# Optimization experiments

Measured on AMD Instinct MI355X. Metric: run time of the kernel, lower is better.

The kernel has to match this reference:

```python
import jax, jax.numpy as jnp
import numpy as np

N_HEAD = 8
D_MODEL = 512
D_K = 512
D_V = 512
D_KH = D_K // N_HEAD
D_VH = D_V // N_HEAD
EPS = 1e-6


def setup_inputs() -> dict:
    key = jax.random.key(0)
    ks = jax.random.split(key, 10)
    B, L = 16, 1024
    q = jax.random.normal(ks[0], (B, L, D_MODEL), dtype=jnp.float32)
    k = jax.random.normal(ks[1], (B, L, D_MODEL), dtype=jnp.float32)
    v = jax.random.normal(ks[2], (B, L, D_MODEL), dtype=jnp.float32)
    mask = jax.random.randint(ks[3], (B, L, L), 0, 2).astype(bool)
    s = 1.0 / np.sqrt(D_MODEL)
    Wq = jax.random.normal(ks[4], (D_MODEL, D_K), dtype=jnp.float32) * s
    Wk = jax.random.normal(ks[5], (D_MODEL, D_K), dtype=jnp.float32) * s
    Wv = jax.random.normal(ks[6], (D_MODEL, D_V), dtype=jnp.float32) * s
    Wfc = jax.random.normal(ks[7], (D_V, D_MODEL), dtype=jnp.float32) * (1.0 / np.sqrt(D_V))
    gamma = jnp.ones((D_MODEL,), dtype=jnp.float32)
    beta = jnp.zeros((D_MODEL,), dtype=jnp.float32)
    return {"q": q, "k": k, "v": v, "mask": mask, "Wq": Wq, "Wk": Wk,
            "Wv": Wv, "Wfc": Wfc, "gamma": gamma, "beta": beta}


def reference(q, k, v, mask, Wq, Wk, Wv, Wfc, gamma, beta):
    B, Lq, _ = q.shape
    Lk = k.shape[1]
    residual = q
    # projections -> [B, H, L, d_head]
    qh = (q @ Wq).reshape(B, Lq, N_HEAD, D_KH).transpose(0, 2, 1, 3)
    kh = (k @ Wk).reshape(B, Lk, N_HEAD, D_KH).transpose(0, 2, 1, 3)
    vh = (v @ Wv).reshape(B, Lk, N_HEAD, D_VH).transpose(0, 2, 1, 3)
    # scaled dot-product attention; scale uses per-head dim (source rebinds d_k)
    scores = jnp.einsum('bhqd,bhkd->bhqk', qh / np.sqrt(D_KH), kh)
    scores = jnp.where(mask[:, None, :, :], -1e9, scores)
    attn = jax.nn.softmax(scores, axis=-1)
    out = jnp.einsum('bhqk,bhkd->bhqd', attn, vh)
    out = out.transpose(0, 2, 1, 3).reshape(B, Lq, D_V)
    out = out @ Wfc + residual
    # layer norm
    mu = jnp.mean(out, axis=-1, keepdims=True)
    var = jnp.var(out, axis=-1, keepdims=True)
    out = (out - mu) * jax.lax.rsqrt(var + EPS) * gamma + beta
    return out, attn
```

## Files before the change

kernel.cpp:

```cpp
#include <hip/hip_runtime.h>
#include <hip/hip_bf16.h>

typedef __attribute__((ext_vector_type(8))) short s8v;
typedef __attribute__((ext_vector_type(4))) short s4v;
typedef __attribute__((ext_vector_type(4))) float f4v;

__device__ __forceinline__ short f2bf(float f){
  unsigned u = __builtin_bit_cast(unsigned, f);
  u += 0x7fffu + ((u >> 16) & 1u);
  return (short)(u >> 16);
}

__device__ __forceinline__ f4v mfma16(s8v a, s8v b, f4v c){
  return __builtin_amdgcn_mfma_f32_16x16x32_bf16(a, b, c, 0, 0, 0);
}

__device__ __forceinline__ void ldsbar(){
  asm volatile("s_waitcnt lgkmcnt(0)" ::: "memory");
  __builtin_amdgcn_s_barrier();
  __builtin_amdgcn_sched_barrier(0);
}

__global__ __launch_bounds__(256) void prep_kernel(
    const int* __restrict__ mask, unsigned* __restrict__ bits,
    const float* __restrict__ Wq, const float* __restrict__ Wk,
    const float* __restrict__ Wv, const float* __restrict__ Wfc,
    short* __restrict__ Wt)
{
  if (blockIdx.x < 2048){
    const int lane = threadIdx.x & 63;
    const int wid = blockIdx.x*4 + (threadIdx.x >> 6);
    for (int i = 0; i < 32; ++i){
      const int c = wid*32 + i;
      int mv = __builtin_nontemporal_load(&mask[(size_t)c*64 + lane]);
      unsigned long long bal = __ballot(mv != 0);
      if (lane == 0)  bits[c*2]   = (unsigned)bal;
      if (lane == 32) bits[c*2+1] = (unsigned)(bal >> 32);
    }
  } else {
    const int bid = blockIdx.x - 2048;
    const int w = bid >> 10;
    const float* __restrict__ W = (w==0)?Wq:(w==1)?Wk:(w==2)?Wv:Wfc;
    const int idx = (bid & 1023)*256 + threadIdx.x;
    const int kk = idx >> 9, n = idx & 511;
    Wt[w*262144 + n*512 + kk] = f2bf(W[idx]);
  }
}

__global__ __launch_bounds__(256) void proj_kernel(
    const float* __restrict__ qin, const float* __restrict__ kin,
    const float* __restrict__ vin, const short* __restrict__ Wt,
    short* __restrict__ Qh, short* __restrict__ Kh, short* __restrict__ Vt)
{
  const int work = (blockIdx.x & 7)*384 + (blockIdx.x >> 3);
  const int z = work >> 10;
  const int r = work & 1023;
  const int mt = r >> 2, nt = r & 3;
  const float* __restrict__ A = (z==0) ? qin : (z==1) ? kin : vin;
  const short* __restrict__ W = Wt + z*262144;
  const int m0 = mt*64, n0 = nt*128;
  __shared__ __align__(16) short Alds[64*40];
  __shared__ __align__(16) short Tlds[128*68];
  const int tid = threadIdx.x, lane = tid & 63, wave = tid >> 6;
  const int wm = wave >> 1, wn = wave & 1;
  const int col = lane & 15, kg = lane >> 4;
  f4v acc[2][4];
  #pragma unroll
  for (int i=0;i<2;i++)
    #pragma unroll
    for (int j=0;j<4;j++) acc[i][j] = (f4v){0.f,0.f,0.f,0.f};

  const int arow = tid >> 2, aoff = (tid & 3)*8;
  const float* Ap = A + (size_t)(m0 + arow)*512 + aoff;
  short* Aw = &Alds[arow*40 + aoff];

  float4 x0 = *(const float4*)(Ap);
  float4 x1 = *(const float4*)(Ap + 4);

  for (int k0 = 0; k0 < 512; k0 += 32){
    s8v ab;
    ab[0]=f2bf(x0.x); ab[1]=f2bf(x0.y); ab[2]=f2bf(x0.z); ab[3]=f2bf(x0.w);
    ab[4]=f2bf(x1.x); ab[5]=f2bf(x1.y); ab[6]=f2bf(x1.z); ab[7]=f2bf(x1.w);
    ldsbar();
    *(s8v*)Aw = ab;
    if (k0 < 480){
      x0 = *(const float4*)(Ap + k0 + 32);
      x1 = *(const float4*)(Ap + k0 + 36);
    }
    ldsbar();
    s8v af0 = *(const s8v*)&Alds[(wm*32 + col)*40 + kg*8];
    s8v af1 = *(const s8v*)&Alds[(wm*32 + 16 + col)*40 + kg*8];
    #pragma unroll
    for (int f=0; f<4; f++){
      const int n = n0 + wn*64 + f*16 + col;
      s8v bf = *(const s8v*)(W + n*512 + k0 + kg*8);
      acc[0][f] = mfma16(af0, bf, acc[0][f]);
      acc[1][f] = mfma16(af1, bf, acc[1][f]);
    }
  }

  if (z < 2){
    const float scale = (z==0) ? 0.125f : 1.0f;
    short* D = (z==0) ? Qh : Kh;
    #pragma unroll
    for (int fr=0; fr<2; fr++)
      #pragma unroll
      for (int f=0; f<4; f++)
        #pragma unroll
        for (int j=0; j<4; j++){
          int rr = m0 + wm*32 + fr*16 + kg*4 + j;
          int c = n0 + wn*64 + f*16 + col;
          int b = rr >> 10, l = rr & 1023, hh = c >> 6, d = c & 63;
          D[((size_t)(b*8+hh)*1024 + l)*64 + d] = f2bf(acc[fr][f][j] * scale);
        }
  } else {
    ldsbar();
    #pragma unroll
    for (int fr=0; fr<2; fr++)
      #pragma unroll
      for (int f=0; f<4; f++)
        #pragma unroll
        for (int j=0; j<4; j++){
          const int rl = wm*32 + fr*16 + kg*4 + j;
          const int cl = wn*64 + f*16 + col;
          Tlds[cl*68 + rl] = f2bf(acc[fr][f][j]);
        }
    ldsbar();
    const int b = m0 >> 10, lbase = m0 & 1023;
    #pragma unroll
    for (int it=0; it<4; ++it){
      const int idx = it*256 + tid;
      const int cl = idx >> 3, rc = idx & 7;
      const int c = n0 + cl, hh = c >> 6, d = c & 63;
      s8v vv = *(const s8v*)&Tlds[cl*68 + rc*8];
      *(s8v*)(Vt + ((size_t)(b*8+hh)*64 + d)*1024 + lbase + rc*8) = vv;
    }
  }
}

__global__ __launch_bounds__(256) void attn_kernel(
  const short* __restrict__ Qh, const short* __restrict__ Kh,
  const short* __restrict__ Vt, const unsigned* __restrict__ bits,
  float* __restrict__ attn, short* __restrict__ ctx)
{
  const int work = ((blockIdx.x & 7) << 8) | (blockIdx.x >> 3);
  const int bh = work >> 4;
  const int q0 = (work & 15) * 64;
  const int b = bh >> 3, h = bh & 7;
  __shared__ unsigned mb[64*33];
  __shared__ __align__(16) short Pb[64*128];
  __shared__ float red[256];
  __shared__ float rowinv[64];
  const int tid = threadIdx.x, lane = tid & 63, wave = tid >> 6;
  const int col = lane & 15, kg = lane >> 4;
  const short* Qb = Qh + (size_t)bh*65536;
  const short* Kb = Kh + (size_t)bh*65536;
  const short* Vb = Vt + (size_t)bh*65536;
  const f4v zf = (f4v){0.f,0.f,0.f,0.f};

  {
    const int r = tid >> 2, w = (tid & 3)*8;
    const unsigned* src = bits + (size_t)(b*1024 + q0 + r)*32 + w;
    uint4 w0 = *(const uint4*)src;
    uint4 w1 = *(const uint4*)(src + 4);
    unsigned* dst = &mb[r*33 + w];
    dst[0]=w0.x; dst[1]=w0.y; dst[2]=w0.z; dst[3]=w0.w;
    dst[4]=w1.x; dst[5]=w1.y; dst[6]=w1.z; dst[7]=w1.w;
  }

  s8v qf[4][2];
  #pragma unroll
  for (int qi = 0; qi < 4; ++qi)
    #pragma unroll
    for (int ks = 0; ks < 2; ++ks)
      qf[qi][ks] = *(const s8v*)(Qb + (q0 + qi*16 + col)*64 + ks*32 + kg*8);

  __syncthreads();

  float sum[4] = {0.f, 0.f, 0.f, 0.f};
  for (int it = 0; it < 8; ++it){
    const int c0 = it*128 + wave*32;
    unsigned mw[4];
    #pragma unroll
    for (int qi = 0; qi < 4; ++qi) mw[qi] = mb[(qi*16 + col)*33 + (c0>>5)];
    #pragma unroll
    for (int ch = 0; ch < 2; ++ch){
      const short* kp = Kb + (c0 + ch*16 + col)*64 + kg*8;
      s8v kf0 = *(const s8v*)kp;
      s8v kf1 = *(const s8v*)(kp + 32);
      #pragma unroll
      for (int qi = 0; qi < 4; ++qi){
        f4v a = mfma16(kf0, qf[qi][0], zf);
        a = mfma16(kf1, qf[qi][1], a);
        #pragma unroll
        for (int j = 0; j < 4; ++j){
          const int bit = ch*16 + kg*4 + j;
          float e = __expf(a[j]);
          sum[qi] += ((mw[qi]>>bit)&1) ? 0.f : e;
        }
      }
    }
  }
  #pragma unroll
  for (int qi = 0; qi < 4; ++qi){
    sum[qi] += __shfl_xor(sum[qi], 16);
    sum[qi] += __shfl_xor(sum[qi], 32);
  }
  if (kg == 0){
    #pragma unroll
    for (int qi = 0; qi < 4; ++qi) red[wave*64 + qi*16 + col] = sum[qi];
  }
  __syncthreads();
  if (tid < 64)
    rowinv[tid] = 1.0f / (red[tid] + red[64+tid] + red[128+tid] + red[192+tid]);
  __syncthreads();
  float inv[4];
  #pragma unroll
  for (int qi = 0; qi < 4; ++qi) inv[qi] = rowinv[qi*16 + col];

  f4v cacc[4] = {zf, zf, zf, zf};
  const int d0 = wave*16;
  float* ab = attn + (size_t)(bh*1024 + q0)*1024;
  const int sw = (col & 7) << 3;
  for (int it = 0; it < 8; ++it){
    const int c0 = it*128 + wave*32;
    unsigned mw[4];
    #pragma unroll
    for (int qi = 0; qi < 4; ++qi) mw[qi] = mb[(qi*16 + col)*33 + (c0>>5)];
    #pragma unroll
    for (int ch = 0; ch < 2; ++ch){
      const int cc = c0 + ch*16;
      const short* kp = Kb + (cc + col)*64 + kg*8;
      s8v kf0 = *(const s8v*)kp;
      s8v kf1 = *(const s8v*)(kp + 32);
      #pragma unroll
      for (int qi = 0; qi < 4; ++qi){
        f4v a = mfma16(kf0, qf[qi][0], zf);
        a = mfma16(kf1, qf[qi][1], a);
        f4v p; s4v pk;
        #pragma unroll
        for (int j = 0; j < 4; ++j){
          const int bit = ch*16 + kg*4 + j;
          float e = __expf(a[j]) * inv[qi];
          p[j] = ((mw[qi]>>bit)&1) ? 0.f : e;
          pk[j] = f2bf(p[j]);
        }
        __builtin_nontemporal_store(p,
            (f4v*)(ab + (size_t)(qi*16 + col)*1024 + cc + kg*4));
        *(s4v*)&Pb[(qi*16 + col)*128 + ((wave*32 + ch*16 + kg*4) ^ sw)] = pk;
      }
    }
    ldsbar();
    #pragma unroll
    for (int sub = 0; sub < 4; ++sub){
      s8v vf = *(const s8v*)(Vb + (size_t)(d0 + col)*1024 + it*128 + sub*32 + kg*8);
      const int kr = (sub*32 + kg*8) ^ sw;
      #pragma unroll
      for (int qi = 0; qi < 4; ++qi){
        s8v pa = *(const s8v*)&Pb[(qi*16 + col)*128 + kr];
        cacc[qi] = mfma16(pa, vf, cacc[qi]);
      }
    }
    ldsbar();
  }

  short* cb = ctx + (size_t)(b*1024 + q0)*512 + h*64 + d0 + col;
  #pragma unroll
  for (int qi = 0; qi < 4; ++qi)
    #pragma unroll
    for (int j = 0; j < 4; ++j)
      cb[(size_t)(qi*16 + kg*4 + j)*512] = f2bf(cacc[qi][j]);
}

__global__ __launch_bounds__(256) void outproj_ln_kernel(
  const short* __restrict__ ctx, const short* __restrict__ Wf,
  const float* __restrict__ resid, const float* __restrict__ gamma,
  const float* __restrict__ beta, float* __restrict__ out)
{
  const int m0 = blockIdx.x * 32;
  __shared__ __align__(16) short Alds[32*40];
  __shared__ float sred[32*4], qred[32*4];
  __shared__ float mLds[32], rLds[32];
  const int tid = threadIdx.x, lane = tid & 63, wave = tid >> 6;
  const int col = lane & 15, kg = lane >> 4;
  const int n0 = wave * 128;

  f4v acc[2][8];
  #pragma unroll
  for (int mf=0; mf<2; mf++)
    #pragma unroll
    for (int nf=0; nf<8; nf++) acc[mf][nf] = (f4v){0.f,0.f,0.f,0.f};

  const int arow = tid >> 3, ac = (tid & 7)*4;
  const short* Ap = ctx + (size_t)(m0 + arow)*512 + ac;
  short* Aw = &Alds[arow*40 + ac];

  s4v av = *(const s4v*)(Ap);

  for (int k0 = 0; k0 < 512; k0 += 32){
    ldsbar();
    *(s4v*)Aw = av;
    if (k0 < 480) av = *(const s4v*)(Ap + k0 + 32);
    ldsbar();
    s8v af[2];
    #pragma unroll
    for (int mf=0; mf<2; mf++)
      af[mf] = *(const s8v*)&Alds[(mf*16 + col)*40 + kg*8];
    #pragma unroll
    for (int nf=0; nf<8; nf++){
      s8v bf = *(const s8v*)(Wf + (size_t)(n0 + nf*16 + col)*512 + k0 + kg*8);
      #pragma unroll
      for (int mf=0; mf<2; mf++)
        acc[mf][nf] = mfma16(af[mf], bf, acc[mf][nf]);
    }
  }

  float g[8], bt[8];
  #pragma unroll
  for (int nf=0; nf<8; nf++){
    g[nf]  = gamma[n0 + nf*16 + col];
    bt[nf] = beta[n0 + nf*16 + col];
  }

  #pragma unroll
  for (int mf=0; mf<2; mf++)
    #pragma unroll
    for (int j=0; j<4; j++){
      const int rl = mf*16 + kg*4 + j;
      const size_t r = (size_t)(m0 + rl);
      float s = 0.f, qq = 0.f;
      #pragma unroll
      for (int nf=0; nf<8; nf++){
        float y = acc[mf][nf][j] + resid[r*512 + n0 + nf*16 + col];
        acc[mf][nf][j] = y;
        s += y; qq += y*y;
      }
      #pragma unroll
      for (int d=1; d<16; d<<=1){ s += __shfl_xor(s, d); qq += __shfl_xor(qq, d); }
      if (col == 0){ sred[rl*4 + wave] = s; qred[rl*4 + wave] = qq; }
    }
  __syncthreads();
  if (tid < 32){
    float S = sred[tid*4] + sred[tid*4+1] + sred[tid*4+2] + sred[tid*4+3];
    float Q = qred[tid*4] + qred[tid*4+1] + qred[tid*4+2] + qred[tid*4+3];
    float mean = S * (1.0f/512.0f);
    float var  = Q * (1.0f/512.0f) - mean*mean;
    mLds[tid] = mean;
    rLds[tid] = rsqrtf(var + 1e-6f);
  }
  __syncthreads();

  #pragma unroll
  for (int mf=0; mf<2; mf++)
    #pragma unroll
    for (int j=0; j<4; j++){
      const int rl = mf*16 + kg*4 + j;
      const size_t r = (size_t)(m0 + rl);
      const float mean = mLds[rl], rs = rLds[rl];
      #pragma unroll
      for (int nf=0; nf<8; nf++)
        out[r*512 + n0 + nf*16 + col] = (acc[mf][nf][j] - mean)*rs*g[nf] + bt[nf];
    }
}

extern "C" void kernel_launch(void* const* d_in, const int* in_sizes, int n_in,
                              void* d_out, int out_size, void* d_ws, size_t ws_size,
                              hipStream_t stream) {
  const float* q    = (const float*)d_in[0];
  const float* k    = (const float*)d_in[1];
  const float* v    = (const float*)d_in[2];
  const int*   mask = (const int*)d_in[3];
  const float* Wq   = (const float*)d_in[4];
  const float* Wk   = (const float*)d_in[5];
  const float* Wv   = (const float*)d_in[6];
  const float* Wfc  = (const float*)d_in[7];
  const float* gamma= (const float*)d_in[8];
  const float* beta = (const float*)d_in[9];

  char* ws = (char*)d_ws;
  short* Wt  = (short*)(ws);
  short* Qh  = (short*)(ws + ((size_t)2<<20));
  short* Kh  = (short*)(ws + ((size_t)18<<20));
  short* Vt  = (short*)(ws + ((size_t)34<<20));
  short* ctx = (short*)(ws + ((size_t)50<<20));

  float* out  = (float*)d_out;
  float* attn = out + (size_t)16384*512;
  unsigned* bits = (unsigned*)d_out;

  prep_kernel<<<dim3(6144,1,1), 256, 0, stream>>>(mask, bits, Wq, Wk, Wv, Wfc, Wt);
  proj_kernel <<<dim3(3072,1,1), 256, 0, stream>>>(q, k, v, Wt, Qh, Kh, Vt);
  attn_kernel <<<dim3(2048,1,1), 256, 0, stream>>>(Qh, Kh, Vt, bits, attn, ctx);
  outproj_ln_kernel<<<dim3(512,1,1), 256, 0, stream>>>(ctx, Wt + 3*262144, q,
                                                       gamma, beta, out);
}
```

Before: 355.9 us.

## Split attention P·V pass by query rows per wave, removing block barriers

The second attention pass now gives each wave its own 16 query rows across all 1024 keys and all 64 output dims. P is staged in a small per-wave LDS tile instead of a shared 64x128 block buffer, so the two block-wide barriers per iteration are gone. The log2(e) factor is folded into the Q projection scale so exp2f can replace __expf. The trade-off is that each wave now reads the full K and V tiles itself, which raises global/L2 traffic per block, and the per-wave LDS write-then-read relies on wave-level ordering without an explicit barrier.

```diff
diff --git a/kernel.cpp b/kernel.cpp
--- a/kernel.cpp
+++ b/kernel.cpp
@@ -20,6 +20,8 @@
   __builtin_amdgcn_s_barrier();
   __builtin_amdgcn_sched_barrier(0);
 }
+
+#define LOG2E 1.44269504088896f
 
 __global__ __launch_bounds__(256) void prep_kernel(
     const int* __restrict__ mask, unsigned* __restrict__ bits,
@@ -100,7 +102,7 @@
   }
 
   if (z < 2){
-    const float scale = (z==0) ? 0.125f : 1.0f;
+    const float scale = (z==0) ? 0.125f*LOG2E : 1.0f;
     short* D = (z==0) ? Qh : Kh;
     #pragma unroll
     for (int fr=0; fr<2; fr++)
@@ -148,7 +150,7 @@
   const int q0 = (work & 15) * 64;
   const int b = bh >> 3, h = bh & 7;
   __shared__ unsigned mb[64*33];
-  __shared__ __align__(16) short Pb[64*128];
+  __shared__ __align__(16) short Pw[4][16][40];
   __shared__ float red[256];
   __shared__ float rowinv[64];
   const int tid = threadIdx.x, lane = tid & 63, wave = tid >> 6;
@@ -195,7 +197,7 @@
         #pragma unroll
         for (int j = 0; j < 4; ++j){
           const int bit = ch*16 + kg*4 + j;
-          float e = __expf(a[j]);
+          float e = exp2f(a[j]);
           sum[qi] += ((mw[qi]>>bit)&1) ? 0.f : e;
         }
       }
@@ -214,62 +216,52 @@
   if (tid < 64)
     rowinv[tid] = 1.0f / (red[tid] + red[64+tid] + red[128+tid] + red[192+tid]);
   __syncthreads();
-  float inv[4];
-  #pragma unroll
-  for (int qi = 0; qi < 4; ++qi) inv[qi] = rowinv[qi*16 + col];
+
+  const int row = wave*16 + col;
+  const float invr = rowinv[row];
+  s8v qb[2];
+  #pragma unroll
+  for (int ks = 0; ks < 2; ++ks)
+    qb[ks] = *(const s8v*)(Qb + (q0 + row)*64 + ks*32 + kg*8);
 
   f4v cacc[4] = {zf, zf, zf, zf};
-  const int d0 = wave*16;
-  float* ab = attn + (size_t)(bh*1024 + q0)*1024;
-  const int sw = (col & 7) << 3;
-  for (int it = 0; it < 8; ++it){
-    const int c0 = it*128 + wave*32;
-    unsigned mw[4];
-    #pragma unroll
-    for (int qi = 0; qi < 4; ++qi) mw[qi] = mb[(qi*16 + col)*33 + (c0>>5)];
+  float* ab = attn + (size_t)(bh*1024 + q0 + row)*1024;
+
+  for (int k0 = 0; k0 < 1024; k0 += 32){
+    const unsigned mw = mb[row*33 + (k0>>5)];
     #pragma unroll
     for (int ch = 0; ch < 2; ++ch){
-      const int cc = c0 + ch*16;
+      const int cc = k0 + ch*16;
       const short* kp = Kb + (cc + col)*64 + kg*8;
       s8v kf0 = *(const s8v*)kp;
       s8v kf1 = *(const s8v*)(kp + 32);
-      #pragma unroll
-      for (int qi = 0; qi < 4; ++qi){
-        f4v a = mfma16(kf0, qf[qi][0], zf);
-        a = mfma16(kf1, qf[qi][1], a);
-        f4v p; s4v pk;
-        #pragma unroll
-        for (int j = 0; j < 4; ++j){
-          const int bit = ch*16 + kg*4 + j;
-          float e = __expf(a[j]) * inv[qi];
-          p[j] = ((mw[qi]>>bit)&1) ? 0.f : e;
-          pk[j] = f2bf(p[j]);
-        }
-        __builtin_nontemporal_store(p,
-            (f4v*)(ab + (size_t)(qi*16 + col)*1024 + cc + kg*4));
-        *(s4v*)&Pb[(qi*16 + col)*128 + ((wave*32 + ch*16 + kg*4) ^ sw)] = pk;
+      f4v a = mfma16(kf0, qb[0], zf);
+      a = mfma16(kf1, qb[1], a);
+      f4v p; s4v pk;
+      #pragma unroll
+      for (int j = 0; j < 4; ++j){
+        const int bit = ch*16 + kg*4 + j;
+        float e = exp2f(a[j]) * invr;
+        p[j] = ((mw>>bit)&1) ? 0.f : e;
+        pk[j] = f2bf(p[j]);
       }
-    }
-    ldsbar();
-    #pragma unroll
-    for (int sub = 0; sub < 4; ++sub){
-      s8v vf = *(const s8v*)(Vb + (size_t)(d0 + col)*1024 + it*128 + sub*32 + kg*8);
-      const int kr = (sub*32 + kg*8) ^ sw;
-      #pragma unroll
-      for (int qi = 0; qi < 4; ++qi){
-        s8v pa = *(const s8v*)&Pb[(qi*16 + col)*128 + kr];
-        cacc[qi] = mfma16(pa, vf, cacc[qi]);
-      }
-    }
-    ldsbar();
-  }
-
-  short* cb = ctx + (size_t)(b*1024 + q0)*512 + h*64 + d0 + col;
-  #pragma unroll
-  for (int qi = 0; qi < 4; ++qi)
+      __builtin_nontemporal_store(p, (f4v*)(ab + cc + kg*4));
+      *(s4v*)&Pw[wave][col][ch*16 + kg*4] = pk;
+    }
+    s8v pa = *(const s8v*)&Pw[wave][col][kg*8];
+    #pragma unroll
+    for (int df = 0; df < 4; ++df){
+      s8v vf = *(const s8v*)(Vb + (size_t)(df*16 + col)*1024 + k0 + kg*8);
+      cacc[df] = mfma16(pa, vf, cacc[df]);
+    }
+  }
+
+  short* cb = ctx + (size_t)(b*1024 + q0 + wave*16)*512 + h*64;
+  #pragma unroll
+  for (int df = 0; df < 4; ++df)
     #pragma unroll
     for (int j = 0; j < 4; ++j)
-      cb[(size_t)(qi*16 + kg*4 + j)*512] = f2bf(cacc[qi][j]);
+      cb[(size_t)(kg*4 + j)*512 + df*16 + col] = f2bf(cacc[df][j]);
 }
 
 __global__ __launch_bounds__(256) void outproj_ln_kernel(
```

Result: slower. 463.1 us (+30.1%).

## Fuse row-sum into PV pass, defer normalization, double-buffer GEMM LDS tiles

Applied to the files above, without the earlier changes.

The attention kernel drops its separate row-sum pass. It accumulates exp values and the unnormalized P·V in one pass, scales the context by the reciprocal row sum at the end, and then recomputes QK^T in a final pass to write the normalized attention matrix. Q is prescaled by log2(e) so the kernel can use exp2f. The projection and output-projection GEMMs double-buffer their LDS A tiles, which removes one barrier per k-step. The overall QK^T compute count stays the same (two passes). The context is now built from unnormalized bf16 probabilities, which may slightly change precision.

```diff
diff --git a/kernel.cpp b/kernel.cpp
--- a/kernel.cpp
+++ b/kernel.cpp
@@ -20,6 +20,8 @@
   __builtin_amdgcn_s_barrier();
   __builtin_amdgcn_sched_barrier(0);
 }
+
+#define LOG2E 1.44269504088896f
 
 __global__ __launch_bounds__(256) void prep_kernel(
     const int* __restrict__ mask, unsigned* __restrict__ bits,
@@ -59,7 +61,7 @@
   const float* __restrict__ A = (z==0) ? qin : (z==1) ? kin : vin;
   const short* __restrict__ W = Wt + z*262144;
   const int m0 = mt*64, n0 = nt*128;
-  __shared__ __align__(16) short Alds[64*40];
+  __shared__ __align__(16) short Alds[2][64*40];
   __shared__ __align__(16) short Tlds[128*68];
   const int tid = threadIdx.x, lane = tid & 63, wave = tid >> 6;
   const int wm = wave >> 1, wn = wave & 1;
@@ -72,24 +74,23 @@
 
   const int arow = tid >> 2, aoff = (tid & 3)*8;
   const float* Ap = A + (size_t)(m0 + arow)*512 + aoff;
-  short* Aw = &Alds[arow*40 + aoff];
 
   float4 x0 = *(const float4*)(Ap);
   float4 x1 = *(const float4*)(Ap + 4);
+  int buf = 0;
 
   for (int k0 = 0; k0 < 512; k0 += 32){
     s8v ab;
     ab[0]=f2bf(x0.x); ab[1]=f2bf(x0.y); ab[2]=f2bf(x0.z); ab[3]=f2bf(x0.w);
     ab[4]=f2bf(x1.x); ab[5]=f2bf(x1.y); ab[6]=f2bf(x1.z); ab[7]=f2bf(x1.w);
-    ldsbar();
-    *(s8v*)Aw = ab;
+    *(s8v*)&Alds[buf][arow*40 + aoff] = ab;
     if (k0 < 480){
       x0 = *(const float4*)(Ap + k0 + 32);
       x1 = *(const float4*)(Ap + k0 + 36);
     }
     ldsbar();
-    s8v af0 = *(const s8v*)&Alds[(wm*32 + col)*40 + kg*8];
-    s8v af1 = *(const s8v*)&Alds[(wm*32 + 16 + col)*40 + kg*8];
+    s8v af0 = *(const s8v*)&Alds[buf][(wm*32 + col)*40 + kg*8];
+    s8v af1 = *(const s8v*)&Alds[buf][(wm*32 + 16 + col)*40 + kg*8];
     #pragma unroll
     for (int f=0; f<4; f++){
       const int n = n0 + wn*64 + f*16 + col;
@@ -97,10 +98,11 @@
       acc[0][f] = mfma16(af0, bf, acc[0][f]);
       acc[1][f] = mfma16(af1, bf, acc[1][f]);
     }
+    buf ^= 1;
   }
 
   if (z < 2){
-    const float scale = (z==0) ? 0.125f : 1.0f;
+    const float scale = (z==0) ? 0.125f*LOG2E : 1.0f;
     short* D = (z==0) ? Qh : Kh;
     #pragma unroll
     for (int fr=0; fr<2; fr++)
@@ -114,7 +116,6 @@
           D[((size_t)(b*8+hh)*1024 + l)*64 + d] = f2bf(acc[fr][f][j] * scale);
         }
   } else {
-    ldsbar();
     #pragma unroll
     for (int fr=0; fr<2; fr++)
       #pragma unroll
@@ -178,49 +179,8 @@
   __syncthreads();
 
   float sum[4] = {0.f, 0.f, 0.f, 0.f};
-  for (int it = 0; it < 8; ++it){
-    const int c0 = it*128 + wave*32;
-    unsigned mw[4];
-    #pragma unroll
-    for (int qi = 0; qi < 4; ++qi) mw[qi] = mb[(qi*16 + col)*33 + (c0>>5)];
-    #pragma unroll
-    for (int ch = 0; ch < 2; ++ch){
-      const short* kp = Kb + (c0 + ch*16 + col)*64 + kg*8;
-      s8v kf0 = *(const s8v*)kp;
-      s8v kf1 = *(const s8v*)(kp + 32);
-      #pragma unroll
-      for (int qi = 0; qi < 4; ++qi){
-        f4v a = mfma16(kf0, qf[qi][0], zf);
-        a = mfma16(kf1, qf[qi][1], a);
-        #pragma unroll
-        for (int j = 0; j < 4; ++j){
-          const int bit = ch*16 + kg*4 + j;
-          float e = __expf(a[j]);
-          sum[qi] += ((mw[qi]>>bit)&1) ? 0.f : e;
-        }
-      }
-    }
-  }
-  #pragma unroll
-  for (int qi = 0; qi < 4; ++qi){
-    sum[qi] += __shfl_xor(sum[qi], 16);
-    sum[qi] += __shfl_xor(sum[qi], 32);
-  }
-  if (kg == 0){
-    #pragma unroll
-    for (int qi = 0; qi < 4; ++qi) red[wave*64 + qi*16 + col] = sum[qi];
-  }
-  __syncthreads();
-  if (tid < 64)
-    rowinv[tid] = 1.0f / (red[tid] + red[64+tid] + red[128+tid] + red[192+tid]);
-  __syncthreads();
-  float inv[4];
-  #pragma unroll
-  for (int qi = 0; qi < 4; ++qi) inv[qi] = rowinv[qi*16 + col];
-
   f4v cacc[4] = {zf, zf, zf, zf};
   const int d0 = wave*16;
-  float* ab = attn + (size_t)(bh*1024 + q0)*1024;
   const int sw = (col & 7) << 3;
   for (int it = 0; it < 8; ++it){
     const int c0 = it*128 + wave*32;
@@ -237,16 +197,15 @@
       for (int qi = 0; qi < 4; ++qi){
         f4v a = mfma16(kf0, qf[qi][0], zf);
         a = mfma16(kf1, qf[qi][1], a);
-        f4v p; s4v pk;
+        s4v pk;
         #pragma unroll
         for (int j = 0; j < 4; ++j){
           const int bit = ch*16 + kg*4 + j;
-          float e = __expf(a[j]) * inv[qi];
-          p[j] = ((mw[qi]>>bit)&1) ? 0.f : e;
-          pk[j] = f2bf(p[j]);
+          float e = exp2f(a[j]);
+          float p = ((mw[qi]>>bit)&1) ? 0.f : e;
+          sum[qi] += p;
+          pk[j] = f2bf(p);
         }
-        __builtin_nontemporal_store(p,
-            (f4v*)(ab + (size_t)(qi*16 + col)*1024 + cc + kg*4));
         *(s4v*)&Pb[(qi*16 + col)*128 + ((wave*32 + ch*16 + kg*4) ^ sw)] = pk;
       }
     }
@@ -264,12 +223,59 @@
     ldsbar();
   }
 
+  #pragma unroll
+  for (int qi = 0; qi < 4; ++qi){
+    sum[qi] += __shfl_xor(sum[qi], 16);
+    sum[qi] += __shfl_xor(sum[qi], 32);
+  }
+  if (kg == 0){
+    #pragma unroll
+    for (int qi = 0; qi < 4; ++qi) red[wave*64 + qi*16 + col] = sum[qi];
+  }
+  __syncthreads();
+  if (tid < 64)
+    rowinv[tid] = 1.0f / (red[tid] + red[64+tid] + red[128+tid] + red[192+tid]);
+  __syncthreads();
+
   short* cb = ctx + (size_t)(b*1024 + q0)*512 + h*64 + d0 + col;
   #pragma unroll
   for (int qi = 0; qi < 4; ++qi)
     #pragma unroll
     for (int j = 0; j < 4; ++j)
-      cb[(size_t)(qi*16 + kg*4 + j)*512] = f2bf(cacc[qi][j]);
+      cb[(size_t)(qi*16 + kg*4 + j)*512] =
+          f2bf(cacc[qi][j] * rowinv[qi*16 + kg*4 + j]);
+
+  float inv[4];
+  #pragma unroll
+  for (int qi = 0; qi < 4; ++qi) inv[qi] = rowinv[qi*16 + col];
+  float* ab = attn + (size_t)(bh*1024 + q0)*1024;
+  for (int it = 0; it < 8; ++it){
+    const int c0 = it*128 + wave*32;
+    unsigned mw[4];
+    #pragma unroll
+    for (int qi = 0; qi < 4; ++qi) mw[qi] = mb[(qi*16 + col)*33 + (c0>>5)];
+    #pragma unroll
+    for (int ch = 0; ch < 2; ++ch){
+      const int cc = c0 + ch*16;
+      const short* kp = Kb + (cc + col)*64 + kg*8;
+      s8v kf0 = *(const s8v*)kp;
+      s8v kf1 = *(const s8v*)(kp + 32);
+      #pragma unroll
+      for (int qi = 0; qi < 4; ++qi){
+        f4v a = mfma16(kf0, qf[qi][0], zf);
+        a = mfma16(kf1, qf[qi][1], a);
+        f4v p;
+        #pragma unroll
+        for (int j = 0; j < 4; ++j){
+          const int bit = ch*16 + kg*4 + j;
+          float e = exp2f(a[j]) * inv[qi];
+          p[j] = ((mw[qi]>>bit)&1) ? 0.f : e;
+        }
+        __builtin_nontemporal_store(p,
+            (f4v*)(ab + (size_t)(qi*16 + col)*1024 + cc + kg*4));
+      }
+    }
+  }
 }
 
 __global__ __launch_bounds__(256) void outproj_ln_kernel(
@@ -278,7 +284,7 @@
   const float* __restrict__ beta, float* __restrict__ out)
 {
   const int m0 = blockIdx.x * 32;
-  __shared__ __align__(16) short Alds[32*40];
+  __shared__ __align__(16) short Alds[2][32*40];
   __shared__ float sred[32*4], qred[32*4];
   __shared__ float mLds[32], rLds[32];
   const int tid = threadIdx.x, lane = tid & 63, wave = tid >> 6;
@@ -293,19 +299,18 @@
 
   const int arow = tid >> 3, ac = (tid & 7)*4;
   const short* Ap = ctx + (size_t)(m0 + arow)*512 + ac;
-  short* Aw = &Alds[arow*40 + ac];
 
   s4v av = *(const s4v*)(Ap);
+  int buf = 0;
 
   for (int k0 = 0; k0 < 512; k0 += 32){
-    ldsbar();
-    *(s4v*)Aw = av;
+    *(s4v*)&Alds[buf][arow*40 + ac] = av;
     if (k0 < 480) av = *(const s4v*)(Ap + k0 + 32);
     ldsbar();
     s8v af[2];
     #pragma unroll
     for (int mf=0; mf<2; mf++)
-      af[mf] = *(const s8v*)&Alds[(mf*16 + col)*40 + kg*8];
+      af[mf] = *(const s8v*)&Alds[buf][(mf*16 + col)*40 + kg*8];
     #pragma unroll
     for (int nf=0; nf<8; nf++){
       s8v bf = *(const s8v*)(Wf + (size_t)(n0 + nf*16 + col)*512 + k0 + kg*8);
@@ -313,6 +318,7 @@
       for (int mf=0; mf<2; mf++)
         acc[mf][nf] = mfma16(af[mf], bf, acc[mf][nf]);
     }
+    buf ^= 1;
   }
 
   float g[8], bt[8];
```

After: 339.1 us. 1.05x faster.
